# Kernel tuning notes

Measured on AMD Instinct MI355X. Metric: run time of the kernel, lower is better.

## Reference

```python
import jax, jax.numpy as jnp
import numpy as np

FP8_E4M3_MAX = 448.0  # max finite value of float8_e4m3fn
ACT_SCALE = 2.0       # self.scale in the torch module
WEIGHT_SCALE = 2.0    # self.weight_scale in the torch module


def qdq_fp8(x, scale):
    """quantize_affine_float8 (clamp + cast to e4m3fn) then dequantize back to f32."""
    q = jnp.clip(x / scale, -FP8_E4M3_MAX, FP8_E4M3_MAX).astype(jnp.float8_e4m3fn)
    return q.astype(jnp.float32) * scale


def setup_inputs() -> dict:
    key = jax.random.key(0)
    k1, k2, k3 = jax.random.split(key, 3)
    x = jax.random.normal(k1, (32, 128, 56, 56), dtype=jnp.float32)
    # weight is stored in fp8 in the torch module; round-trip through fp8 so the
    # f32 tensor holds exactly representable fp8 values.
    w = jax.random.normal(k2, (256, 128, 3, 3), dtype=jnp.float32)
    w = w.astype(jnp.float8_e4m3fn).astype(jnp.float32)
    b = jax.random.normal(k3, (256,), dtype=jnp.float32)
    return {"input": x, "weight": w, "bias": b}


def reference(input, weight, bias):
    # dequantize fp8 weight: cast-to-f32 already done in setup, apply scale
    w = weight * WEIGHT_SCALE
    # quantize + dequantize the activation through fp8 e4m3
    dq_input = qdq_fp8(input, ACT_SCALE)
    out = jax.lax.conv_general_dilated(
        dq_input, w,
        window_strides=(1, 1),
        padding=[(1, 1), (1, 1)],
        lhs_dilation=(1, 1),
        rhs_dilation=(1, 1),  # dilation=1
        dimension_numbers=("NCHW", "OIHW", "NCHW"),
        feature_group_count=1,
    )
    return out + bias[None, :, None, None]
```

## Files before the change

kernel.cpp:

```cpp
#include <hip/hip_runtime.h>
#include <cstdint>


#define NB   32
#define CIN  128
#define HW   56
#define KOUT 256

#define ACT_BYTES (32u * 56u * 56u * 128u)
#define WT_OFF    ACT_BYTES
#define WT_BYTES  (9u * 256u * 128u)
#define ZP_OFF    (WT_OFF + WT_BYTES)

typedef float        f32x4 __attribute__((ext_vector_type(4)));
typedef unsigned int u32x4 __attribute__((ext_vector_type(4)));

__device__ __forceinline__ unsigned int pack2_fp8(float a, float b) {
  a = fminf(fmaxf(a, -448.f), 448.f);
  b = fminf(fmaxf(b, -448.f), 448.f);
  return (unsigned int)__builtin_amdgcn_cvt_pk_fp8_f32(a, b, 0, false);
}

__global__ __launch_bounds__(256) void qdq_pack(const float* __restrict__ X,
                                                unsigned char* __restrict__ act) {
  const int nh = blockIdx.x;
  const int n = nh / HW, h = nh - n * HW;
  const float* xb = X + (size_t)n * (CIN * HW * HW) + h * HW;
  unsigned char* ob = act + (size_t)nh * (HW * CIN);

  for (int i = 0; i < 2; ++i) {
    int item = threadIdx.x + i * 256;
    if (item >= HW * 8) break;
    int w = item % HW, cg = item / HW;
    unsigned int dw[4];
#pragma unroll
    for (int jj = 0; jj < 4; ++jj) {
      int c0 = cg * 16 + jj * 4;
      float v0 = xb[(c0 + 0) * 3136 + w] * 0.5f;
      float v1 = xb[(c0 + 1) * 3136 + w] * 0.5f;
      float v2 = xb[(c0 + 2) * 3136 + w] * 0.5f;
      float v3 = xb[(c0 + 3) * 3136 + w] * 0.5f;
      unsigned int lo = pack2_fp8(v0, v1) & 0xffffu;
      unsigned int hi = pack2_fp8(v2, v3) & 0xffffu;
      dw[jj] = lo | (hi << 16);
    }
    u32x4 v = {dw[0], dw[1], dw[2], dw[3]};
    *(u32x4*)(ob + w * CIN + cg * 16) = v;
  }
}

__global__ __launch_bounds__(256) void pack_weight(const float* __restrict__ W,
                                                   unsigned char* __restrict__ wt,
                                                   unsigned int* __restrict__ zp) {
  if (blockIdx.x == 0 && threadIdx.x < 32) zp[threadIdx.x] = 0u;
  int gid = blockIdx.x * 256 + threadIdx.x;
  int o = gid * 4;
  if (o >= (int)WT_BYTES) return;
  int rs = o >> 15;
  int rem = o & 32767;
  int k  = rem >> 7;
  int c0 = rem & 127;
  float v0 = W[k * 1152 + (c0 + 0) * 9 + rs];
  float v1 = W[k * 1152 + (c0 + 1) * 9 + rs];
  float v2 = W[k * 1152 + (c0 + 2) * 9 + rs];
  float v3 = W[k * 1152 + (c0 + 3) * 9 + rs];
  unsigned int dw = (pack2_fp8(v0, v1) & 0xffffu) | (pack2_fp8(v2, v3) << 16);
  *(unsigned int*)(wt + o) = dw;
}

__device__ __forceinline__ void g2l16(const void* g, void* l) {
  __builtin_amdgcn_global_load_lds((const __attribute__((address_space(1))) void*)g,
                                   (__attribute__((address_space(3))) void*)l,
                                   16, 0, 0);
}

__global__ __launch_bounds__(256) void conv_mfma(const unsigned char* __restrict__ act,
                                                 const unsigned char* __restrict__ wt,
                                                 const unsigned char* __restrict__ zp,
                                                 const float* __restrict__ bias,
                                                 float* __restrict__ out) {
  __shared__ __align__(16) unsigned char lds[32768];
  const int tid  = threadIdx.x;
  const int lane = tid & 63;
  const int wid  = tid >> 6;
  const int wr   = wid >> 1, wc = wid & 1;
  const int bm   = blockIdx.x << 7;
  const int bn   = blockIdx.y << 7;

  const int srow   = tid >> 3;
  const int sphys  = (tid & 7) << 4;
  const int schunk = ((tid & 7) ^ (srow & 7)) << 4;

  int an_[4], ah_[4], aw_[4];
#pragma unroll
  for (int q = 0; q < 4; ++q) {
    int m = bm + srow + 32 * q;
    int n = m / 3136;
    int hw = m - n * 3136;
    int h = hw / 56;
    an_[q] = n; ah_[q] = h; aw_[q] = hw - h * 56;
  }

  const f32x4 zero = {0.f, 0.f, 0.f, 0.f};
  f32x4 acc[4][4];
#pragma unroll
  for (int i = 0; i < 4; ++i)
#pragma unroll
    for (int j = 0; j < 4; ++j) acc[i][j] = zero;

  for (int rs = 0; rs < 9; ++rs) {
    const int r = rs / 3, s = rs - 3 * (rs / 3);
    const unsigned char* wseg = wt + rs * (KOUT * CIN);

#pragma unroll
    for (int q = 0; q < 4; ++q) {
      int hi = ah_[q] + r - 1;
      int wi = aw_[q] + s - 1;
      bool ok = ((unsigned)hi < 56u) && ((unsigned)wi < 56u);
      const unsigned char* src =
          ok ? act + (((an_[q] * 56 + hi) * 56 + wi) << 7) + schunk : zp + schunk;
      g2l16(src, &lds[((srow + 32 * q) << 7) + sphys]);
    }
#pragma unroll
    for (int q = 0; q < 4; ++q) {
      int kl = srow + 32 * q;
      g2l16(wseg + ((bn + kl) << 7) + schunk, &lds[16384 + (kl << 7) + sphys]);
    }
    __syncthreads();

    const int kgrp = (lane >> 4) << 3;
    const int xa   = (lane & 7) << 4;
#pragma unroll
    for (int kk = 0; kk < 4; ++kk) {
      const int kb = kk * 32 + kgrp;
      long av[4], bv[4];
#pragma unroll
      for (int mi = 0; mi < 4; ++mi) {
        int row = (wr << 6) + (mi << 4) + (lane & 15);
        av[mi] = *(const long*)(&lds[(row << 7) + (kb ^ xa)]);
      }
#pragma unroll
      for (int ni = 0; ni < 4; ++ni) {
        int col = (wc << 6) + (ni << 4) + (lane & 15);
        bv[ni] = *(const long*)(&lds[16384 + (col << 7) + (kb ^ xa)]);
      }
#pragma unroll
      for (int mi = 0; mi < 4; ++mi)
#pragma unroll
        for (int ni = 0; ni < 4; ++ni)
          acc[mi][ni] = __builtin_amdgcn_mfma_f32_16x16x32_fp8_fp8(
              av[mi], bv[ni], acc[mi][ni], 0, 0, 0);
    }
    __syncthreads();
  }

#pragma unroll
  for (int ni = 0; ni < 4; ++ni) {
    int k = bn + (wc << 6) + (ni << 4) + (lane & 15);
    float bvv = bias[k];
#pragma unroll
    for (int mi = 0; mi < 4; ++mi) {
      int m = bm + (wr << 6) + (mi << 4) + ((lane >> 4) << 2);
      int n = m / 3136;
      int hw = m - n * 3136;
      f32x4 v = acc[mi][ni];
      v = v * 4.0f + bvv;
      *(f32x4*)(out + (size_t)(n * KOUT + k) * 3136 + hw) = v;
    }
  }
}

extern "C" void kernel_launch(void* const* d_in, const int* in_sizes, int n_in,
                              void* d_out, int out_size, void* d_ws, size_t ws_size,
                              hipStream_t stream) {
  const float* X = (const float*)d_in[0];
  const float* W = (const float*)d_in[1];
  const float* B = (const float*)d_in[2];
  float* out = (float*)d_out;

  unsigned char* act = (unsigned char*)d_ws;
  unsigned char* wtb = act + WT_OFF;
  unsigned char* zp  = act + ZP_OFF;

  hipLaunchKernelGGL(qdq_pack,    dim3(NB * HW), dim3(256), 0, stream, X, act);
  hipLaunchKernelGGL(pack_weight, dim3(288),     dim3(256), 0, stream, W, wtb,
                     (unsigned int*)zp);
  hipLaunchKernelGGL(conv_mfma,   dim3(784, 2),  dim3(256), 0, stream, act, wtb, zp, B,
                     out);
}
```

Measured before the change: 82.77 us.

## Double-buffer LDS with 256x128 tiles and interleaved prefetch in FP8 conv

The conv kernel now uses 512-thread blocks covering 256 output pixels by 128 channels. The A and B tiles are double-buffered in LDS, and loads for the next filter tap are issued in slices between the MFMA sub-steps. Block indices are remapped so that consecutive blocks land on spread-out M tiles, and s_setprio raises priority around the MFMA bursts. This is meant to hide global-to-LDS latency and reuse each weight tile across more rows, at the cost of 96KB of LDS per block (which limits occupancy) and more barriers per tap.

Result: slower. 108.2 us (+30.7%).

```diff
diff --git a/kernel.cpp b/kernel.cpp
--- a/kernel.cpp
+++ b/kernel.cpp
@@ -6,6 +6,7 @@
 #define CIN  128
 #define HW   56
 #define KOUT 256
+#define MTOT (32 * 56 * 56)
 
 #define ACT_BYTES (32u * 56u * 56u * 128u)
 #define WT_OFF    ACT_BYTES
@@ -74,18 +75,22 @@
                                    16, 0, 0);
 }
 
-__global__ __launch_bounds__(256) void conv_mfma(const unsigned char* __restrict__ act,
+__global__ __launch_bounds__(512) void conv_mfma(const unsigned char* __restrict__ act,
                                                  const unsigned char* __restrict__ wt,
                                                  const unsigned char* __restrict__ zp,
                                                  const float* __restrict__ bias,
                                                  float* __restrict__ out) {
-  __shared__ __align__(16) unsigned char lds[32768];
+  __shared__ __align__(16) unsigned char ldsA[2][32768];
+  __shared__ __align__(16) unsigned char ldsB[2][16384];
   const int tid  = threadIdx.x;
   const int lane = tid & 63;
   const int wid  = tid >> 6;
   const int wr   = wid >> 1, wc = wid & 1;
-  const int bm   = blockIdx.x << 7;
-  const int bn   = blockIdx.y << 7;
+
+  const int bx  = (int)blockIdx.x;
+  const int bmi = (bx & 7) * 49 + (bx >> 3);
+  const int bm  = bmi << 8;
+  const int bn  = (int)blockIdx.y << 7;
 
   const int srow   = tid >> 3;
   const int sphys  = (tid & 7) << 4;
@@ -94,64 +99,92 @@
   int an_[4], ah_[4], aw_[4];
 #pragma unroll
   for (int q = 0; q < 4; ++q) {
-    int m = bm + srow + 32 * q;
+    int m = bm + srow + 64 * q;
     int n = m / 3136;
     int hw = m - n * 3136;
     int h = hw / 56;
     an_[q] = n; ah_[q] = h; aw_[q] = hw - h * 56;
   }
 
-  const f32x4 zero = {0.f, 0.f, 0.f, 0.f};
-  f32x4 acc[4][4];
-#pragma unroll
-  for (int i = 0; i < 4; ++i)
-#pragma unroll
-    for (int j = 0; j < 4; ++j) acc[i][j] = zero;
-
-  for (int rs = 0; rs < 9; ++rs) {
-    const int r = rs / 3, s = rs - 3 * (rs / 3);
-    const unsigned char* wseg = wt + rs * (KOUT * CIN);
-
-#pragma unroll
-    for (int q = 0; q < 4; ++q) {
+  auto stageA2 = [&](unsigned char* bufA, int r, int s, int q0) {
+#pragma unroll
+    for (int q = q0; q < q0 + 2; ++q) {
       int hi = ah_[q] + r - 1;
       int wi = aw_[q] + s - 1;
       bool ok = ((unsigned)hi < 56u) && ((unsigned)wi < 56u);
       const unsigned char* src =
           ok ? act + (((an_[q] * 56 + hi) * 56 + wi) << 7) + schunk : zp + schunk;
-      g2l16(src, &lds[((srow + 32 * q) << 7) + sphys]);
-    }
-#pragma unroll
-    for (int q = 0; q < 4; ++q) {
-      int kl = srow + 32 * q;
-      g2l16(wseg + ((bn + kl) << 7) + schunk, &lds[16384 + (kl << 7) + sphys]);
-    }
-    __syncthreads();
-
-    const int kgrp = (lane >> 4) << 3;
-    const int xa   = (lane & 7) << 4;
-#pragma unroll
-    for (int kk = 0; kk < 4; ++kk) {
-      const int kb = kk * 32 + kgrp;
+      g2l16(src, bufA + ((srow + 64 * q) << 7) + sphys);
+    }
+  };
+  auto stageB2 = [&](unsigned char* bufB, int rs) {
+    const unsigned char* wseg = wt + rs * (KOUT * CIN);
+#pragma unroll
+    for (int q = 0; q < 2; ++q) {
+      int kl = srow + 64 * q;
+      g2l16(wseg + ((bn + kl) << 7) + schunk, bufB + (kl << 7) + sphys);
+    }
+  };
+
+  const f32x4 zero = {0.f, 0.f, 0.f, 0.f};
+  f32x4 acc[4][4];
+#pragma unroll
+  for (int i = 0; i < 4; ++i)
+#pragma unroll
+    for (int j = 0; j < 4; ++j) acc[i][j] = zero;
+
+  stageA2(ldsA[0], 0, 0, 0);
+  stageA2(ldsA[0], 0, 0, 2);
+  stageB2(ldsB[0], 0);
+  __builtin_amdgcn_sched_barrier(0);
+  asm volatile("s_waitcnt vmcnt(0)" ::: "memory");
+  __builtin_amdgcn_s_barrier();
+
+  const int xa = (lane & 7) << 4;
+  for (int t = 0; t < 9; ++t) {
+    const int rn = (t + 1) / 3, sn = (t + 1) - 3 * rn;
+    const unsigned char* bA = ldsA[t & 1];
+    const unsigned char* bB = ldsB[t & 1];
+    unsigned char* nA = ldsA[(t + 1) & 1];
+    unsigned char* nB = ldsB[(t + 1) & 1];
+
+#pragma unroll
+    for (int P = 0; P < 4; ++P) {
+      const int kb = (P << 5) + ((lane >> 4) << 3);
       long av[4], bv[4];
 #pragma unroll
       for (int mi = 0; mi < 4; ++mi) {
         int row = (wr << 6) + (mi << 4) + (lane & 15);
-        av[mi] = *(const long*)(&lds[(row << 7) + (kb ^ xa)]);
+        av[mi] = *(const long*)(bA + (row << 7) + (kb ^ xa));
       }
 #pragma unroll
       for (int ni = 0; ni < 4; ++ni) {
         int col = (wc << 6) + (ni << 4) + (lane & 15);
-        bv[ni] = *(const long*)(&lds[16384 + (col << 7) + (kb ^ xa)]);
-      }
+        bv[ni] = *(const long*)(bB + (col << 7) + (kb ^ xa));
+      }
+      if (t < 8) {
+        if (P == 0)      stageA2(nA, rn, sn, 0);
+        else if (P == 1) stageA2(nA, rn, sn, 2);
+        else if (P == 2) stageB2(nB, t + 1);
+      }
+      __builtin_amdgcn_sched_barrier(0);
+      __builtin_amdgcn_s_barrier();
+      asm volatile("s_waitcnt lgkmcnt(0)" ::: "memory");
+      __builtin_amdgcn_sched_barrier(0);
+      __builtin_amdgcn_s_setprio(1);
 #pragma unroll
       for (int mi = 0; mi < 4; ++mi)
 #pragma unroll
         for (int ni = 0; ni < 4; ++ni)
           acc[mi][ni] = __builtin_amdgcn_mfma_f32_16x16x32_fp8_fp8(
               av[mi], bv[ni], acc[mi][ni], 0, 0, 0);
-    }
-    __syncthreads();
+      __builtin_amdgcn_s_setprio(0);
+      if (P == 3) {
+        __builtin_amdgcn_sched_barrier(0);
+        asm volatile("s_waitcnt vmcnt(0)" ::: "memory");
+      }
+      __builtin_amdgcn_s_barrier();
+    }
   }
 
 #pragma unroll
@@ -185,6 +218,6 @@
   hipLaunchKernelGGL(qdq_pack,    dim3(NB * HW), dim3(256), 0, stream, X, act);
   hipLaunchKernelGGL(pack_weight, dim3(288),     dim3(256), 0, stream, W, wtb,
                      (unsigned int*)zp);
-  hipLaunchKernelGGL(conv_mfma,   dim3(784, 2),  dim3(256), 0, stream, act, wtb, zp, B,
+  hipLaunchKernelGGL(conv_mfma,   dim3(392, 2),  dim3(512), 0, stream, act, wtb, zp, B,
                      out);
 }
```
